# Kernel optimization log

Measured on AMD Instinct MI355X. Metric: run time of the kernel, lower is better.

Reference implementation:

```python
import jax, jax.numpy as jnp
import numpy as np

H = 16  # num_heads


def rope_cos_sin(S, d):
    # interleaved RoPE tables: cos = [cos0,cos0,cos1,cos1,...], sin likewise
    pos = jnp.arange(S, dtype=jnp.float32)[:, None]            # [S,1]
    ids = jnp.arange(d // 2, dtype=jnp.float32)
    theta = jnp.power(10000.0, -2.0 * ids / d)                  # [d/2]
    ang = pos * theta                                           # [S,d/2]
    cos = jnp.repeat(jnp.cos(ang), 2, axis=-1)                  # [S,d]
    sin = jnp.repeat(jnp.sin(ang), 2, axis=-1)                  # [S,d]
    return cos, sin


def apply_rope(x, cos, sin):
    # x: [B,H,S,d]; x2 = [-x1, x0, -x3, x2, ...]
    x2 = jnp.stack([-x[..., 1::2], x[..., ::2]], axis=-1).reshape(x.shape)
    return x * cos + x2 * sin


def setup_inputs() -> dict:
    key = jax.random.key(0)
    ks = jax.random.split(key, 9)
    B, S, D = 2, 2048, 1024
    sc = 1.0 / np.sqrt(D)
    return {
        "x": jax.random.normal(ks[0], (B, S, D), dtype=jnp.float32),
        "Wq": jax.random.normal(ks[1], (D, D), dtype=jnp.float32) * sc,
        "bq": jnp.zeros((D,), dtype=jnp.float32),
        "Wk": jax.random.normal(ks[2], (D, D), dtype=jnp.float32) * sc,
        "bk": jnp.zeros((D,), dtype=jnp.float32),
        "Wv": jax.random.normal(ks[3], (D, D), dtype=jnp.float32) * sc,
        "bv": jnp.zeros((D,), dtype=jnp.float32),
        "Wo": jax.random.normal(ks[4], (D, D), dtype=jnp.float32) * sc,
        "bo": jnp.zeros((D,), dtype=jnp.float32),
    }


def reference(x, Wq, bq, Wk, bk, Wv, bv, Wo, bo):
    B, S, D = x.shape
    dk = D // H
    scale = dk ** -0.5  # lsa=False -> fixed scale
    # QKV projections -> [B,H,S,dk]
    q = (x @ Wq + bq).reshape(B, S, H, dk).transpose(0, 2, 1, 3)
    k = (x @ Wk + bk).reshape(B, S, H, dk).transpose(0, 2, 1, 3)
    v = (x @ Wv + bv).reshape(B, S, H, dk).transpose(0, 2, 1, 3)
    cos, sin = rope_cos_sin(S, dk)
    q = apply_rope(q, cos, sin)
    k = apply_rope(k, cos, sin)
    attn_scores = jnp.einsum('bhqd,bhkd->bhqk', q, k) * scale
    attn_weights = jax.nn.softmax(attn_scores, axis=-1)  # dropout p=0
    out = jnp.einsum('bhqk,bhkd->bhqd', attn_weights, v)
    out = out.transpose(0, 2, 1, 3).reshape(B, S, D)
    out = out @ Wo + bo
    return out, attn_weights
```

## Files before the change

kernel.cpp:

```cpp
#include <hip/hip_runtime.h>

typedef __attribute__((ext_vector_type(4))) float f32x4;
typedef __attribute__((ext_vector_type(4))) int   i32x4;
typedef __attribute__((ext_vector_type(8))) short bf16x8;
typedef __attribute__((ext_vector_type(4))) short s16x4;

#define HD 16
#define SQ 2048
#define DM 1024
#define DK 64
#define QSCALE 0.18033688011112042f

__device__ __forceinline__ short f2bf(float f){
  union { float f; unsigned u; } c; c.f = f;
  unsigned r = (c.u + 0x7FFFu + ((c.u >> 16) & 1u)) >> 16;
  return (short)r;
}
__device__ __forceinline__ f32x4 mfma16(bf16x8 a, bf16x8 b, f32x4 c){
  return __builtin_amdgcn_mfma_f32_16x16x32_bf16(a, b, c, 0, 0, 0);
}
__device__ __forceinline__ void gload16(const void* g, void* l){
  __builtin_amdgcn_global_load_lds(
      (const __attribute__((address_space(1))) unsigned*)g,
      (__attribute__((address_space(3))) unsigned*)l, 16, 0, 0);
}


__global__ void k_rope_tab(float2* __restrict__ tab){
  int i = blockIdx.x * 256 + threadIdx.x;
  int s = i >> 5, d2 = i & 31;
  float theta = powf(10000.0f, -(float)d2 / 32.0f);
  float ang = (float)s * theta;
  tab[i] = make_float2(cosf(ang), sinf(ang));
}

__global__ void k_cast(const float* __restrict__ x, short* __restrict__ xb){
  int i = (blockIdx.x * 256 + threadIdx.x) * 4;
  f32x4 v = *(const f32x4*)(x + i);
  s16x4 o;
  o[0] = f2bf(v[0]); o[1] = f2bf(v[1]); o[2] = f2bf(v[2]); o[3] = f2bf(v[3]);
  *(s16x4*)(xb + i) = o;
}

__global__ void k_wt4(const float* __restrict__ W0, const float* __restrict__ W1,
                      const float* __restrict__ W2, const float* __restrict__ W3,
                      short* __restrict__ T0, short* __restrict__ T1,
                      short* __restrict__ T2, short* __restrict__ T3){
  __shared__ float t[32][33];
  const float* W; short* Wt;
  if (blockIdx.z == 0)      { W = W0; Wt = T0; }
  else if (blockIdx.z == 1) { W = W1; Wt = T1; }
  else if (blockIdx.z == 2) { W = W2; Wt = T2; }
  else                      { W = W3; Wt = T3; }
  int kx = blockIdx.x * 32, nx = blockIdx.y * 32;
  int lx = threadIdx.x & 31, ly = threadIdx.x >> 5;
#pragma unroll
  for (int i = 0; i < 32; i += 8)
    t[ly + i][lx] = W[(size_t)(kx + ly + i) * DM + nx + lx];
  __syncthreads();
#pragma unroll
  for (int i = 0; i < 32; i += 8)
    Wt[(size_t)(nx + ly + i) * DM + kx + lx] = f2bf(t[lx][ly + i]);
}

__global__ __launch_bounds__(256) void k_projqkv(const short* __restrict__ A,
    const short* __restrict__ Wqt, const short* __restrict__ Wkt, const short* __restrict__ Wvt,
    const float* __restrict__ bq, const float* __restrict__ bk, const float* __restrict__ bv,
    const float2* __restrict__ rope,
    short* __restrict__ Qo, short* __restrict__ Ko, short* __restrict__ Vo)
{
  __shared__ short As[128 * 64];
  __shared__ short Bs[128 * 64];
  const int mat = blockIdx.y >> 3;
  const int n0 = (blockIdx.y & 7) * 128;
  const short* Bt  = (mat == 0) ? Wqt : (mat == 1) ? Wkt : Wvt;
  const float* bias = (mat == 0) ? bq : (mat == 1) ? bk : bv;
  const int tid = threadIdx.x;
  const int lane = tid & 63, w = tid >> 6;
  const int wr = w >> 1, wc = w & 1;
  const int l15 = lane & 15, l4 = lane >> 4;
  const int m0 = blockIdx.x * 128;
  f32x4 acc[4][4] = {};

  for (int k0 = 0; k0 < DM; k0 += 64) {
#pragma unroll
    for (int i = 0; i < 4; ++i) {
      int c = w * 4 + i;
      int row = c * 8 + (lane >> 3);
      int so = (((lane & 7) * 16) ^ ((row & 7) << 4)) >> 1;
      gload16(A  + (size_t)(m0 + row) * DM + k0 + so, (char*)As + c * 1024);
      gload16(Bt + (size_t)(n0 + row) * DM + k0 + so, (char*)Bs + c * 1024);
    }
    __syncthreads();
#pragma unroll
    for (int kk = 0; kk < 64; kk += 32) {
      bf16x8 af[4], bfr[4];
#pragma unroll
      for (int mi = 0; mi < 4; ++mi) {
        int r = wr * 64 + mi * 16 + l15;
        af[mi] = *(const bf16x8*)((char*)As + ((r * 128 + kk * 2 + l4 * 16) ^ ((r & 7) << 4)));
      }
#pragma unroll
      for (int ni = 0; ni < 4; ++ni) {
        int r = wc * 64 + ni * 16 + l15;
        bfr[ni] = *(const bf16x8*)((char*)Bs + ((r * 128 + kk * 2 + l4 * 16) ^ ((r & 7) << 4)));
      }
#pragma unroll
      for (int mi = 0; mi < 4; ++mi)
#pragma unroll
        for (int ni = 0; ni < 4; ++ni)
          acc[mi][ni] = mfma16(af[mi], bfr[ni], acc[mi][ni]);
    }
    __syncthreads();
  }

#pragma unroll
  for (int mi = 0; mi < 4; ++mi) {
#pragma unroll
    for (int ni = 0; ni < 4; ++ni) {
      int n = n0 + wc * 64 + ni * 16 + l15;
      float bv2 = bias[n];
      if (mat == 2) {
        s16x4 pk;
        int mb = m0 + wr * 64 + mi * 16 + l4 * 4;
#pragma unroll
        for (int r2 = 0; r2 < 4; ++r2) pk[r2] = f2bf(acc[mi][ni][r2] + bv2);
        int b = mb >> 11, s = mb & 2047, h = n >> 6, d = n & 63;
        *(s16x4*)(Vo + ((size_t)((b * HD + h) * DK + d)) * SQ + s) = pk;
      } else {
        short* outp = (mat == 0) ? Qo : Ko;
        float sc = (mat == 0) ? QSCALE : 1.0f;
#pragma unroll
        for (int r2 = 0; r2 < 4; ++r2) {
          int m = m0 + wr * 64 + mi * 16 + l4 * 4 + r2;
          float v = acc[mi][ni][r2] + bv2;
          float pr = __shfl_xor(v, 1);
          int s = m & 2047, d = n & 63;
          float2 cs = rope[(s << 5) + (d >> 1)];
          v = (d & 1) ? (v * cs.x + pr * cs.y) : (v * cs.x - pr * cs.y);
          v *= sc;
          int b = m >> 11, h = n >> 6;
          outp[((size_t)((b * HD + h) * SQ + s)) * DK + d] = f2bf(v);
        }
      }
    }
  }
}

__global__ __launch_bounds__(256) void k_projO(const short* __restrict__ A, const short* __restrict__ Bt,
                                               const float* __restrict__ bias, float* __restrict__ out)
{
  __shared__ short As[64 * 64];
  __shared__ short Bs[128 * 64];
  const int tid = threadIdx.x;
  const int lane = tid & 63, w = tid >> 6;
  const int wr = w >> 1, wc = w & 1;
  const int l15 = lane & 15, l4 = lane >> 4;
  const int m0 = blockIdx.x * 64, n0 = blockIdx.y * 128;
  f32x4 acc[2][4] = {};

  for (int k0 = 0; k0 < DM; k0 += 64) {
#pragma unroll
    for (int i = 0; i < 2; ++i) {
      int c = w * 2 + i;
      int row = c * 8 + (lane >> 3);
      int so = (((lane & 7) * 16) ^ ((row & 7) << 4)) >> 1;
      gload16(A + (size_t)(m0 + row) * DM + k0 + so, (char*)As + c * 1024);
    }
#pragma unroll
    for (int i = 0; i < 4; ++i) {
      int c = w * 4 + i;
      int row = c * 8 + (lane >> 3);
      int so = (((lane & 7) * 16) ^ ((row & 7) << 4)) >> 1;
      gload16(Bt + (size_t)(n0 + row) * DM + k0 + so, (char*)Bs + c * 1024);
    }
    __syncthreads();
#pragma unroll
    for (int kk = 0; kk < 64; kk += 32) {
      bf16x8 af[2], bfr[4];
#pragma unroll
      for (int mi = 0; mi < 2; ++mi) {
        int r = wr * 32 + mi * 16 + l15;
        af[mi] = *(const bf16x8*)((char*)As + ((r * 128 + kk * 2 + l4 * 16) ^ ((r & 7) << 4)));
      }
#pragma unroll
      for (int ni = 0; ni < 4; ++ni) {
        int r = wc * 64 + ni * 16 + l15;
        bfr[ni] = *(const bf16x8*)((char*)Bs + ((r * 128 + kk * 2 + l4 * 16) ^ ((r & 7) << 4)));
      }
#pragma unroll
      for (int mi = 0; mi < 2; ++mi)
#pragma unroll
        for (int ni = 0; ni < 4; ++ni)
          acc[mi][ni] = mfma16(af[mi], bfr[ni], acc[mi][ni]);
    }
    __syncthreads();
  }

#pragma unroll
  for (int mi = 0; mi < 2; ++mi)
#pragma unroll
    for (int ni = 0; ni < 4; ++ni) {
      int n = n0 + wc * 64 + ni * 16 + l15;
      float bv2 = bias[n];
#pragma unroll
      for (int r2 = 0; r2 < 4; ++r2) {
        int m = m0 + wr * 32 + mi * 16 + l4 * 4 + r2;
        out[(size_t)m * DM + n] = acc[mi][ni][r2] + bv2;
      }
    }
}

__global__ __launch_bounds__(256, 4) void k_attn2(const short* __restrict__ Q, const short* __restrict__ K,
    const short* __restrict__ Vt, float* __restrict__ attn_out, short* __restrict__ ctx)
{
  __shared__ short Kbuf[2][64 * 64];
  __shared__ short Vbuf[2][64 * 64];
  __shared__ short Psb[4][16 * 64];
  const int idx = blockIdx.x;
  const int xcd = idx & 7, g = idx >> 3;
  const int bh = xcd * 4 + (g >> 5);
  const int qt = g & 31;
  const int tid = threadIdx.x, lane = tid & 63, w = tid >> 6;
  const int l15 = lane & 15, l4 = lane >> 4;
  const short* Qg = Q + (size_t)(bh * SQ + qt * 64) * DK;
  const short* Kg = K + (size_t)bh * SQ * DK;
  const short* Vg = Vt + (size_t)bh * DK * SQ;
  char* Pw = (char*)Psb[w];

  const int c0 = w * 2, c1 = w * 2 + 1;
  const int row0 = c0 * 8 + (lane >> 3), row1 = c1 * 8 + (lane >> 3);
  const int so0 = (((lane & 7) * 16) ^ ((row0 & 7) << 4)) >> 1;
  const int so1 = (((lane & 7) * 16) ^ ((row1 & 7) << 4)) >> 1;

  bf16x8 q_b[2];
#pragma unroll
  for (int kx = 0; kx < 2; ++kx)
    q_b[kx] = *(const bf16x8*)(Qg + (w * 16 + l15) * 64 + kx * 32 + l4 * 8);

  gload16(Kg + (size_t)row0 * 64 + so0, (char*)Kbuf[0] + c0 * 1024);
  gload16(Kg + (size_t)row1 * 64 + so1, (char*)Kbuf[0] + c1 * 1024);
  __syncthreads();
  float rs = 0.0f;
  for (int t = 0; t < 32; ++t) {
    int cur = t & 1;
    if (t < 31) {
      gload16(Kg + (size_t)((t + 1) * 64 + row0) * 64 + so0, (char*)Kbuf[cur ^ 1] + c0 * 1024);
      gload16(Kg + (size_t)((t + 1) * 64 + row1) * 64 + so1, (char*)Kbuf[cur ^ 1] + c1 * 1024);
    }
    const char* Kc = (const char*)Kbuf[cur];
#pragma unroll
    for (int ni = 0; ni < 4; ++ni) {
      f32x4 p = {};
#pragma unroll
      for (int kx = 0; kx < 2; ++kx) {
        int r = ni * 16 + l15;
        bf16x8 ka = *(const bf16x8*)(Kc + ((r * 128 + kx * 64 + l4 * 16) ^ ((r & 7) << 4)));
        p = mfma16(ka, q_b[kx], p);
      }
#pragma unroll
      for (int r2 = 0; r2 < 4; ++r2) rs += exp2f(p[r2]);
    }
    __syncthreads();
  }
  float rv = rs;
  rv += __shfl_xor(rv, 16);
  rv += __shfl_xor(rv, 32);
  const float rinv = 1.0f / rv;

  f32x4 c[4] = {};
  float* attn_base = attn_out + ((size_t)(bh * SQ + qt * 64)) * SQ;

  gload16(Kg + (size_t)row0 * 64 + so0, (char*)Kbuf[0] + c0 * 1024);
  gload16(Kg + (size_t)row1 * 64 + so1, (char*)Kbuf[0] + c1 * 1024);
  gload16(Vg + (size_t)row0 * SQ + so0, (char*)Vbuf[0] + c0 * 1024);
  gload16(Vg + (size_t)row1 * SQ + so1, (char*)Vbuf[0] + c1 * 1024);
  __syncthreads();
  for (int t = 0; t < 32; ++t) {
    int cur = t & 1;
    if (t < 31) {
      gload16(Kg + (size_t)((t + 1) * 64 + row0) * 64 + so0, (char*)Kbuf[cur ^ 1] + c0 * 1024);
      gload16(Kg + (size_t)((t + 1) * 64 + row1) * 64 + so1, (char*)Kbuf[cur ^ 1] + c1 * 1024);
      gload16(Vg + (size_t)row0 * SQ + (t + 1) * 64 + so0, (char*)Vbuf[cur ^ 1] + c0 * 1024);
      gload16(Vg + (size_t)row1 * SQ + (t + 1) * 64 + so1, (char*)Vbuf[cur ^ 1] + c1 * 1024);
    }
    const char* Kc = (const char*)Kbuf[cur];
    const char* Vc = (const char*)Vbuf[cur];
#pragma unroll
    for (int ni = 0; ni < 4; ++ni) {
      f32x4 p = {};
#pragma unroll
      for (int kx = 0; kx < 2; ++kx) {
        int r = ni * 16 + l15;
        bf16x8 ka = *(const bf16x8*)(Kc + ((r * 128 + kx * 64 + l4 * 16) ^ ((r & 7) << 4)));
        p = mfma16(ka, q_b[kx], p);
      }
      f32x4 wv;
      s16x4 pk;
#pragma unroll
      for (int r2 = 0; r2 < 4; ++r2) {
        wv[r2] = exp2f(p[r2]) * rinv;
        pk[r2] = f2bf(wv[r2]);
      }
      *(f32x4*)(attn_base + (size_t)(w * 16 + l15) * SQ + t * 64 + ni * 16 + l4 * 4) = wv;
      *(s16x4*)(Pw + ((l15 * 128 + ni * 32 + l4 * 8) ^ ((l15 & 7) << 4))) = pk;
    }
#pragma unroll
    for (int kk = 0; kk < 64; kk += 32) {
      bf16x8 ap = *(const bf16x8*)(Pw + ((l15 * 128 + kk * 2 + l4 * 16) ^ ((l15 & 7) << 4)));
#pragma unroll
      for (int nd = 0; nd < 4; ++nd) {
        int r = nd * 16 + l15;
        bf16x8 bv = *(const bf16x8*)(Vc + ((r * 128 + kk * 2 + l4 * 16) ^ ((r & 7) << 4)));
        c[nd] = mfma16(ap, bv, c[nd]);
      }
    }
    __syncthreads();
  }
  int b = bh >> 4, h = bh & 15;
#pragma unroll
  for (int nd = 0; nd < 4; ++nd)
#pragma unroll
    for (int r2 = 0; r2 < 4; ++r2) {
      int s = qt * 64 + w * 16 + l4 * 4 + r2;
      int d = nd * 16 + l15;
      ctx[((size_t)(b * SQ + s)) * DM + h * DK + d] = f2bf(c[nd][r2]);
    }
}

extern "C" void kernel_launch(void* const* d_in, const int* in_sizes, int n_in,
                              void* d_out, int out_size, void* d_ws, size_t ws_size,
                              hipStream_t stream)
{
  const float* x  = (const float*)d_in[0];
  const float* Wq = (const float*)d_in[1];
  const float* bq = (const float*)d_in[2];
  const float* Wk = (const float*)d_in[3];
  const float* bk = (const float*)d_in[4];
  const float* Wv = (const float*)d_in[5];
  const float* bv = (const float*)d_in[6];
  const float* Wo = (const float*)d_in[7];
  const float* bo = (const float*)d_in[8];

  char* p = (char*)d_ws;
  float2* rope = (float2*)p;  p += (size_t)SQ * 32 * sizeof(float2);
  short* xb  = (short*)p;     p += (size_t)4096 * DM * 2;
  short* Wqt = (short*)p;     p += (size_t)DM * DM * 2;
  short* Wkt = (short*)p;     p += (size_t)DM * DM * 2;
  short* Wvt = (short*)p;     p += (size_t)DM * DM * 2;
  short* Wot = (short*)p;     p += (size_t)DM * DM * 2;
  short* Qr  = (short*)p;     p += (size_t)2 * HD * SQ * DK * 2;
  short* Kr  = (short*)p;     p += (size_t)2 * HD * SQ * DK * 2;
  short* Vtr = (short*)p;     p += (size_t)2 * HD * SQ * DK * 2;
  short* ctx = (short*)p;     p += (size_t)4096 * DM * 2;

  k_rope_tab<<<SQ * 32 / 256, 256, 0, stream>>>(rope);
  k_cast<<<4096 * DM / 1024, 256, 0, stream>>>(x, xb);
  k_wt4<<<dim3(32, 32, 4), 256, 0, stream>>>(Wq, Wk, Wv, Wo, Wqt, Wkt, Wvt, Wot);
  k_projqkv<<<dim3(32, 24), 256, 0, stream>>>(xb, Wqt, Wkt, Wvt, bq, bk, bv, rope, Qr, Kr, Vtr);
  float* attn = (float*)d_out + (size_t)2 * SQ * DM;
  k_attn2<<<1024, 256, 0, stream>>>(Qr, Kr, Vtr, attn, ctx);
  k_projO<<<dim3(64, 8), 256, 0, stream>>>(ctx, Wot, bo, (float*)d_out);
}
```

Measured before the change: 292.3 us.

## Split attention waves 2x2 over query and key halves to reuse K fragments

Re-partitions the four waves of the attention kernel from one 16-row query strip each into a 2x2 grid: each wave handles 32 query rows and 32 of the 64 keys per tile. Each K fragment loaded from LDS now feeds two query sub-tiles, which cuts LDS reads per MFMA. The cost is extra cross-wave work: the softmax row sums and the PV partial outputs must be combined through shared memory, and the P tile becomes one shared 64x64 buffer instead of per-wave buffers.

```diff
diff --git a/kernel.cpp b/kernel.cpp
--- a/kernel.cpp
+++ b/kernel.cpp
@@ -216,32 +216,34 @@
 {
   __shared__ short Kbuf[2][64 * 64];
   __shared__ short Vbuf[2][64 * 64];
-  __shared__ short Psb[4][16 * 64];
+  __shared__ short Ps[64 * 64];
   const int idx = blockIdx.x;
   const int xcd = idx & 7, g = idx >> 3;
   const int bh = xcd * 4 + (g >> 5);
   const int qt = g & 31;
   const int tid = threadIdx.x, lane = tid & 63, w = tid >> 6;
   const int l15 = lane & 15, l4 = lane >> 4;
+  const int qg = w >> 1, kg = w & 1;
   const short* Qg = Q + (size_t)(bh * SQ + qt * 64) * DK;
   const short* Kg = K + (size_t)bh * SQ * DK;
   const short* Vg = Vt + (size_t)bh * DK * SQ;
-  char* Pw = (char*)Psb[w];
 
   const int c0 = w * 2, c1 = w * 2 + 1;
   const int row0 = c0 * 8 + (lane >> 3), row1 = c1 * 8 + (lane >> 3);
   const int so0 = (((lane & 7) * 16) ^ ((row0 & 7) << 4)) >> 1;
   const int so1 = (((lane & 7) * 16) ^ ((row1 & 7) << 4)) >> 1;
 
-  bf16x8 q_b[2];
-#pragma unroll
-  for (int kx = 0; kx < 2; ++kx)
-    q_b[kx] = *(const bf16x8*)(Qg + (w * 16 + l15) * 64 + kx * 32 + l4 * 8);
+  bf16x8 q_b[2][2];
+#pragma unroll
+  for (int qs = 0; qs < 2; ++qs)
+#pragma unroll
+    for (int kx = 0; kx < 2; ++kx)
+      q_b[qs][kx] = *(const bf16x8*)(Qg + (qg * 32 + qs * 16 + l15) * 64 + kx * 32 + l4 * 8);
 
   gload16(Kg + (size_t)row0 * 64 + so0, (char*)Kbuf[0] + c0 * 1024);
   gload16(Kg + (size_t)row1 * 64 + so1, (char*)Kbuf[0] + c1 * 1024);
   __syncthreads();
-  float rs = 0.0f;
+  float rs[2] = {0.0f, 0.0f};
   for (int t = 0; t < 32; ++t) {
     int cur = t & 1;
     if (t < 31) {
@@ -249,26 +251,49 @@
       gload16(Kg + (size_t)((t + 1) * 64 + row1) * 64 + so1, (char*)Kbuf[cur ^ 1] + c1 * 1024);
     }
     const char* Kc = (const char*)Kbuf[cur];
-#pragma unroll
-    for (int ni = 0; ni < 4; ++ni) {
-      f32x4 p = {};
+    bf16x8 af[2][2];
+#pragma unroll
+    for (int ks = 0; ks < 2; ++ks)
 #pragma unroll
       for (int kx = 0; kx < 2; ++kx) {
-        int r = ni * 16 + l15;
-        bf16x8 ka = *(const bf16x8*)(Kc + ((r * 128 + kx * 64 + l4 * 16) ^ ((r & 7) << 4)));
-        p = mfma16(ka, q_b[kx], p);
-      }
-#pragma unroll
-      for (int r2 = 0; r2 < 4; ++r2) rs += exp2f(p[r2]);
-    }
-    __syncthreads();
-  }
-  float rv = rs;
-  rv += __shfl_xor(rv, 16);
-  rv += __shfl_xor(rv, 32);
-  const float rinv = 1.0f / rv;
-
-  f32x4 c[4] = {};
+        int r = kg * 32 + ks * 16 + l15;
+        af[ks][kx] = *(const bf16x8*)(Kc + ((r * 128 + kx * 64 + l4 * 16) ^ ((r & 7) << 4)));
+      }
+#pragma unroll
+    for (int qs = 0; qs < 2; ++qs)
+#pragma unroll
+      for (int ks = 0; ks < 2; ++ks) {
+        f32x4 p = {};
+        p = mfma16(af[ks][0], q_b[qs][0], p);
+        p = mfma16(af[ks][1], q_b[qs][1], p);
+#pragma unroll
+        for (int r2 = 0; r2 < 4; ++r2) rs[qs] += exp2f(p[r2]);
+      }
+    __syncthreads();
+  }
+  float rv[2];
+#pragma unroll
+  for (int qs = 0; qs < 2; ++qs) {
+    float v = rs[qs];
+    v += __shfl_xor(v, 16);
+    v += __shfl_xor(v, 32);
+    rv[qs] = v;
+  }
+  {
+    float* rst = (float*)Ps;
+    if (lane < 16) {
+#pragma unroll
+      for (int qs = 0; qs < 2; ++qs)
+        rst[(((qg * 2 + qs) * 16 + l15) * 2) + kg] = rv[qs];
+    }
+    __syncthreads();
+#pragma unroll
+    for (int qs = 0; qs < 2; ++qs)
+      rv[qs] = 1.0f / (rv[qs] + rst[(((qg * 2 + qs) * 16 + l15) * 2) + (kg ^ 1)]);
+  }
+  const float rinv0 = rv[0], rinv1 = rv[1];
+
+  f32x4 c[2][4] = {};
   float* attn_base = attn_out + ((size_t)(bh * SQ + qt * 64)) * SQ;
 
   gload16(Kg + (size_t)row0 * 64 + so0, (char*)Kbuf[0] + c0 * 1024);
@@ -286,46 +311,72 @@
     }
     const char* Kc = (const char*)Kbuf[cur];
     const char* Vc = (const char*)Vbuf[cur];
-#pragma unroll
-    for (int ni = 0; ni < 4; ++ni) {
-      f32x4 p = {};
+    bf16x8 af[2][2];
+#pragma unroll
+    for (int ks = 0; ks < 2; ++ks)
 #pragma unroll
       for (int kx = 0; kx < 2; ++kx) {
-        int r = ni * 16 + l15;
-        bf16x8 ka = *(const bf16x8*)(Kc + ((r * 128 + kx * 64 + l4 * 16) ^ ((r & 7) << 4)));
-        p = mfma16(ka, q_b[kx], p);
-      }
-      f32x4 wv;
-      s16x4 pk;
-#pragma unroll
-      for (int r2 = 0; r2 < 4; ++r2) {
-        wv[r2] = exp2f(p[r2]) * rinv;
-        pk[r2] = f2bf(wv[r2]);
-      }
-      *(f32x4*)(attn_base + (size_t)(w * 16 + l15) * SQ + t * 64 + ni * 16 + l4 * 4) = wv;
-      *(s16x4*)(Pw + ((l15 * 128 + ni * 32 + l4 * 8) ^ ((l15 & 7) << 4))) = pk;
-    }
-#pragma unroll
-    for (int kk = 0; kk < 64; kk += 32) {
-      bf16x8 ap = *(const bf16x8*)(Pw + ((l15 * 128 + kk * 2 + l4 * 16) ^ ((l15 & 7) << 4)));
-#pragma unroll
-      for (int nd = 0; nd < 4; ++nd) {
-        int r = nd * 16 + l15;
-        bf16x8 bv = *(const bf16x8*)(Vc + ((r * 128 + kk * 2 + l4 * 16) ^ ((r & 7) << 4)));
-        c[nd] = mfma16(ap, bv, c[nd]);
-      }
-    }
-    __syncthreads();
-  }
-  int b = bh >> 4, h = bh & 15;
-#pragma unroll
-  for (int nd = 0; nd < 4; ++nd)
-#pragma unroll
-    for (int r2 = 0; r2 < 4; ++r2) {
-      int s = qt * 64 + w * 16 + l4 * 4 + r2;
-      int d = nd * 16 + l15;
-      ctx[((size_t)(b * SQ + s)) * DM + h * DK + d] = f2bf(c[nd][r2]);
-    }
+        int r = kg * 32 + ks * 16 + l15;
+        af[ks][kx] = *(const bf16x8*)(Kc + ((r * 128 + kx * 64 + l4 * 16) ^ ((r & 7) << 4)));
+      }
+#pragma unroll
+    for (int qs = 0; qs < 2; ++qs) {
+      const float rinv = qs ? rinv1 : rinv0;
+#pragma unroll
+      for (int ks = 0; ks < 2; ++ks) {
+        f32x4 p = {};
+        p = mfma16(af[ks][0], q_b[qs][0], p);
+        p = mfma16(af[ks][1], q_b[qs][1], p);
+        f32x4 wv;
+        s16x4 pk;
+#pragma unroll
+        for (int r2 = 0; r2 < 4; ++r2) {
+          wv[r2] = exp2f(p[r2]) * rinv;
+          pk[r2] = f2bf(wv[r2]);
+        }
+        int qr = qg * 32 + qs * 16 + l15;
+        *(f32x4*)(attn_base + (size_t)qr * SQ + t * 64 + kg * 32 + ks * 16 + l4 * 4) = wv;
+        *(s16x4*)((char*)Ps + ((qr * 128 + kg * 64 + ks * 32 + l4 * 8) ^ ((qr & 7) << 4))) = pk;
+      }
+    }
+#pragma unroll
+    for (int qs = 0; qs < 2; ++qs) {
+      int qr = qg * 32 + qs * 16 + l15;
+      bf16x8 ap = *(const bf16x8*)((char*)Ps + ((qr * 128 + kg * 64 + l4 * 16) ^ ((qr & 7) << 4)));
+#pragma unroll
+      for (int ds = 0; ds < 4; ++ds) {
+        int r = ds * 16 + l15;
+        bf16x8 bv = *(const bf16x8*)(Vc + ((r * 128 + kg * 64 + l4 * 16) ^ ((r & 7) << 4)));
+        c[qs][ds] = mfma16(ap, bv, c[qs][ds]);
+      }
+    }
+    __syncthreads();
+  }
+  float* red = (float*)Kbuf;
+  if (kg == 1) {
+#pragma unroll
+    for (int qs = 0; qs < 2; ++qs)
+#pragma unroll
+      for (int ds = 0; ds < 4; ++ds)
+#pragma unroll
+        for (int r2 = 0; r2 < 4; ++r2)
+          red[(qg * 32 + qs * 16 + l4 * 4 + r2) * 64 + ds * 16 + l15] = c[qs][ds][r2];
+  }
+  __syncthreads();
+  if (kg == 0) {
+    int b = bh >> 4, h = bh & 15;
+#pragma unroll
+    for (int qs = 0; qs < 2; ++qs)
+#pragma unroll
+      for (int ds = 0; ds < 4; ++ds)
+#pragma unroll
+        for (int r2 = 0; r2 < 4; ++r2) {
+          int qr = qg * 32 + qs * 16 + l4 * 4 + r2;
+          float v = c[qs][ds][r2] + red[qr * 64 + ds * 16 + l15];
+          int s = qt * 64 + qr, d = ds * 16 + l15;
+          ctx[((size_t)(b * SQ + s)) * DM + h * DK + d] = f2bf(v);
+        }
+  }
 }
 
 extern "C" void kernel_launch(void* const* d_in, const int* in_sizes, int n_in,
```

Measured after the change: 283.1 us. 3.1% less time.
